# Kernel optimization log

Hardware: AMD Instinct MI355X
Metric: run time of the kernel (lower is better)

## Reference

```python
import jax, jax.numpy as jnp
import numpy as np

RNN_SIZE = 256
FC_DIM = 64
IMG_DIM = 3200
EMB_DIM = 300


def setup_inputs() -> dict:
    key = jax.random.key(0)
    ks = jax.random.split(key, 16)
    n, L = 64, 512
    s = 0.02
    return {
        "img_feats": jax.random.normal(ks[0], (n, L, IMG_DIM), jnp.float32),
        "phrase_emb": jax.random.normal(ks[1], (n, EMB_DIM), jnp.float32),
        "masks": jnp.ones((n, L), jnp.float32),
        "select_ixs": jax.random.randint(ks[2], (n,), 0, L),
        # cnn_fc_layer: Linear(3200 -> 64)
        "W_cnn": jax.random.normal(ks[3], (IMG_DIM, FC_DIM), jnp.float32) * s,
        "b_cnn": jnp.zeros((FC_DIM,), jnp.float32),
        # phrase_embed: Linear(300 -> 64)
        "W_phr": jax.random.normal(ks[4], (EMB_DIM, FC_DIM), jnp.float32) * s,
        "b_phr": jnp.zeros((FC_DIM,), jnp.float32),
        # LSTMCell(64 -> 256), gate order i,f,g,o as in torch
        "W_ih": jax.random.normal(ks[5], (FC_DIM, 4 * RNN_SIZE), jnp.float32) * s,
        "b_ih": jnp.zeros((4 * RNN_SIZE,), jnp.float32),
        "W_hh": jax.random.normal(ks[6], (RNN_SIZE, 4 * RNN_SIZE), jnp.float32) * s,
        "b_hh": jnp.zeros((4 * RNN_SIZE,), jnp.float32),
        # classifier: Linear(256 -> 64) -> ReLU -> Linear(64 -> 2) -> LogSoftmax
        "W_c1": jax.random.normal(ks[7], (RNN_SIZE, FC_DIM), jnp.float32) * s,
        "b_c1": jnp.zeros((FC_DIM,), jnp.float32),
        "W_c2": jax.random.normal(ks[8], (FC_DIM, 2), jnp.float32) * s,
        "b_c2": jnp.zeros((2,), jnp.float32),
    }


def _forward(img_feats, phrase_emb, select_ixs,
             W_cnn, b_cnn, W_phr, b_phr,
             W_ih, b_ih, W_hh, b_hh,
             W_c1, b_c1, W_c2, b_c2):
    n, L, _ = img_feats.shape
    # per-step small FCs, vectorized over time (dropout is inference no-op)
    img_fc = jax.nn.relu(jnp.einsum('nld,df->nlf', img_feats, W_cnn) + b_cnn)  # (n,L,64)
    emb = jax.nn.relu(phrase_emb @ W_phr + b_phr)                               # (n,64)
    fuse = img_fc * emb[:, None, :]                                             # (n,L,64)

    def cell(carry, x_t):
        h, c = carry
        gates = x_t @ W_ih + b_ih + h @ W_hh + b_hh        # (n, 4*H)
        i, f, g, o = jnp.split(gates, 4, axis=-1)
        i, f, o = jax.nn.sigmoid(i), jax.nn.sigmoid(f), jax.nn.sigmoid(o)
        g = jnp.tanh(g)
        c = f * c + i * g
        h = o * jnp.tanh(c)
        return (h, c), h

    h0 = jnp.zeros((n, RNN_SIZE), fuse.dtype)
    c0 = jnp.zeros((n, RNN_SIZE), fuse.dtype)
    _, hs = jax.lax.scan(cell, (h0, c0), jnp.swapaxes(fuse, 0, 1))  # (L,n,H)
    output_feats = jnp.swapaxes(hs, 0, 1)                           # (n,L,H)

    hid = jax.nn.relu(jnp.einsum('nlh,hf->nlf', output_feats, W_c1) + b_c1)
    logits = jnp.einsum('nlf,fk->nlk', hid, W_c2) + b_c2
    logprobs = jax.nn.log_softmax(logits, axis=-1)                  # (n,L,2)

    selected = jnp.take_along_axis(output_feats, select_ixs[:, None, None], axis=1)[:, 0, :]
    return logprobs, output_feats, selected


def reference(img_feats, phrase_emb, masks, select_ixs,
              W_cnn, b_cnn, W_phr, b_phr,
              W_ih, b_ih, W_hh, b_hh,
              W_c1, b_c1, W_c2, b_c2):
    # masks is accepted but unused, as in the original forward()
    return _forward(img_feats, phrase_emb, select_ixs,
                    W_cnn, b_cnn, W_phr, b_phr,
                    W_ih, b_ih, W_hh, b_hh,
                    W_c1, b_c1, W_c2, b_c2)
```

## Files before the change

### kernel.cpp

```cpp
#include <hip/hip_runtime.h>
#include <hip/hip_bf16.h>
#include <stdint.h>

#define LSEQ 512
#define NB   64
#define IMGD 3200
#define EMBD 300
#define HD   256

typedef __bf16 bf16x8 __attribute__((ext_vector_type(8)));
typedef float  f32x4  __attribute__((ext_vector_type(4)));

__device__ __forceinline__ unsigned short f2bf(float x) {
  unsigned u = __builtin_bit_cast(unsigned, x);
  u = (u + 0x7FFFu + ((u >> 16) & 1u)) >> 16;
  return (unsigned short)u;
}

__global__ __launch_bounds__(256) void k1_init_emb(
    const float* __restrict__ phr, const float* __restrict__ Wp,
    const float* __restrict__ bp, float* __restrict__ emb,
    unsigned* __restrict__ hbuf) {
  int tid = threadIdx.x, blk = blockIdx.x;
  int gid = blk * 256 + tid;
  if (gid < 16384)
    hbuf[gid] = 0u;
  if (blk < 16) {
    int b = gid >> 6, f = gid & 63;
    float acc = bp[f];
    for (int k = 0; k < EMBD; ++k) acc += phr[b * EMBD + k] * Wp[k * 64 + f];
    emb[gid] = fmaxf(acc, 0.f);
  }
}

__global__ __launch_bounds__(256) void k2_imgfuse(
    const float* __restrict__ img, const float* __restrict__ Wc,
    const float* __restrict__ bc, const float* __restrict__ emb,
    unsigned short* __restrict__ fuse) {
  __shared__ float sX[32 * 65];
  __shared__ float sW[64 * 64];
  int tid = threadIdx.x, blk = blockIdx.x;
  int r = tid & 31, g = tid >> 5;
  int rs = tid >> 3, cs = (tid & 7) * 8;
  float acc[8];
#pragma unroll
  for (int j = 0; j < 8; ++j) acc[j] = 0.f;

  for (int k0 = 0; k0 < IMGD; k0 += 64) {
    const float* xsrc = img + (size_t)(blk * 32 + rs) * IMGD + k0 + cs;
    float4 v0 = *(const float4*)xsrc;
    float4 v1 = *(const float4*)(xsrc + 4);
    float* xd = sX + rs * 65 + cs;
    xd[0]=v0.x; xd[1]=v0.y; xd[2]=v0.z; xd[3]=v0.w;
    xd[4]=v1.x; xd[5]=v1.y; xd[6]=v1.z; xd[7]=v1.w;
    const float4* wsrc = (const float4*)(Wc + k0 * 64);
#pragma unroll
    for (int i = 0; i < 4; ++i) ((float4*)sW)[i * 256 + tid] = wsrc[i * 256 + tid];
    __syncthreads();
#pragma unroll 8
    for (int k = 0; k < 64; ++k) {
      float xv = sX[r * 65 + k];
      const float* wr = sW + k * 64 + g * 8;
      float4 wa = *(const float4*)wr;
      float4 wb = *(const float4*)(wr + 4);
      acc[0] += xv * wa.x; acc[1] += xv * wa.y; acc[2] += xv * wa.z; acc[3] += xv * wa.w;
      acc[4] += xv * wb.x; acc[5] += xv * wb.y; acc[6] += xv * wb.z; acc[7] += xv * wb.w;
    }
    __syncthreads();
  }
  int rowg = blk * 32 + r;
  int b = rowg >> 9;
  unsigned pk[4];
#pragma unroll
  for (int j2 = 0; j2 < 4; ++j2) {
    int c = g * 8 + j2 * 2;
    float v0 = fmaxf(acc[j2 * 2] + bc[c], 0.f) * emb[b * 64 + c];
    float v1 = fmaxf(acc[j2 * 2 + 1] + bc[c + 1], 0.f) * emb[b * 64 + c + 1];
    pk[j2] = (unsigned)f2bf(v0) | ((unsigned)f2bf(v1) << 16);
  }
  *(uint4*)(fuse + (size_t)rowg * 64 + g * 8) = make_uint4(pk[0], pk[1], pk[2], pk[3]);
}

__global__ __launch_bounds__(256) void k3_lstm(
    const float* __restrict__ Wih, const float* __restrict__ bih,
    const float* __restrict__ Whh, const float* __restrict__ bhh,
    const unsigned short* __restrict__ fuse,
    unsigned* __restrict__ hbuf, float* __restrict__ outfeats) {
  __shared__ __align__(16) unsigned short sZ[16 * 328];
  int tid = threadIdx.x;
  int wg  = blockIdx.x;
  int grp = wg >> 4;
  int j16 = wg & 15;
  int b0  = grp * 16;
  int h0  = j16 * 16;
  int w = tid >> 6, l = tid & 63;
  int q = l >> 4, c = l & 15;

  int gcol = (c >> 2) * 256 + h0 + w * 4 + (c & 3);
  bf16x8 Bf[10];
#pragma unroll
  for (int kk = 0; kk < 10; ++kk) {
#pragma unroll
    for (int j = 0; j < 8; ++j) {
      int k = kk * 32 + q * 8 + j;
      float v = (k < 256) ? Whh[k * 1024 + gcol] : Wih[(k - 256) * 1024 + gcol];
      Bf[kk][j] = __builtin_bit_cast(__bf16, f2bf(v));
    }
  }
  float bv = bih[gcol] + bhh[gcol];

  int row = tid >> 4, u16i = tid & 15;
  const unsigned short* fbase = fuse + ((size_t)(b0 + row) * 512) * 64 + u16i * 4;
  unsigned short* zh = sZ + row * 328 + u16i * 16;
  unsigned short* zx = sZ + row * 328 + 256 + u16i * 4;
  const unsigned short* za = sZ + c * 328 + q * 8;

  int batch = (q << 2) + ((l >> 2) & 3);
  int ug = h0 + ((w << 2) | (l & 3));
  float* obase = outfeats + ((size_t)(b0 + batch) * 512) * 256 + ug;
  unsigned* mbase = hbuf + (size_t)(b0 + batch) * 256 + ug;
  float cst = 0.f;

  for (int step = 0; step < LSEQ; ++step) {
    uint2 fv = *(const uint2*)(fbase + (size_t)step * 64);
    __syncthreads();
    const unsigned long long* pb =
        (const unsigned long long*)(hbuf + (step & 1) * 16384 +
                                    (b0 + row) * 256 + u16i * 16);
    unsigned long long want = (unsigned long long)(step & 0xFFFF);
    unsigned long long m[8];
    for (;;) {
      bool ok = true;
#pragma unroll
      for (int i = 0; i < 8; ++i)
        m[i] = __hip_atomic_load(pb + i, __ATOMIC_RELAXED, __HIP_MEMORY_SCOPE_AGENT);
#pragma unroll
      for (int i = 0; i < 8; ++i)
        ok = ok && (((m[i] >> 16) & 0xFFFFull) == want) && ((m[i] >> 48) == want);
      if (ok) break;
      __builtin_amdgcn_s_sleep(1);
    }
    unsigned o0 = (unsigned)((m[0] & 0xFFFFull) | ((m[0] >> 16) & 0xFFFF0000ull));
    unsigned o1 = (unsigned)((m[1] & 0xFFFFull) | ((m[1] >> 16) & 0xFFFF0000ull));
    unsigned o2 = (unsigned)((m[2] & 0xFFFFull) | ((m[2] >> 16) & 0xFFFF0000ull));
    unsigned o3 = (unsigned)((m[3] & 0xFFFFull) | ((m[3] >> 16) & 0xFFFF0000ull));
    unsigned o4 = (unsigned)((m[4] & 0xFFFFull) | ((m[4] >> 16) & 0xFFFF0000ull));
    unsigned o5 = (unsigned)((m[5] & 0xFFFFull) | ((m[5] >> 16) & 0xFFFF0000ull));
    unsigned o6 = (unsigned)((m[6] & 0xFFFFull) | ((m[6] >> 16) & 0xFFFF0000ull));
    unsigned o7 = (unsigned)((m[7] & 0xFFFFull) | ((m[7] >> 16) & 0xFFFF0000ull));
    ((uint4*)zh)[0] = make_uint4(o0, o1, o2, o3);
    ((uint4*)zh)[1] = make_uint4(o4, o5, o6, o7);
    *(uint2*)zx = fv;
    __syncthreads();
    f32x4 acc = {bv, bv, bv, bv};
#pragma unroll
    for (int kk = 0; kk < 10; ++kk) {
      bf16x8 a = *(const bf16x8*)(za + kk * 32);
      acc = __builtin_amdgcn_mfma_f32_16x16x32_bf16(a, Bf[kk], acc, 0, 0, 0);
    }
    int g0 = (l >> 2) & 1, g1 = (l >> 3) & 1;
    float v0 = acc[0], v1 = acc[1], v2 = acc[2], v3 = acc[3];
    float s0 = __shfl_xor(v1, 4), s1 = __shfl_xor(v0, 4);
    float s2 = __shfl_xor(v3, 4), s3 = __shfl_xor(v2, 4);
    float y0 = (g0 == 0) ? v0 : s0;
    float y1 = (g0 == 1) ? v1 : s1;
    float y2 = (g0 == 0) ? v2 : s2;
    float y3 = (g0 == 1) ? v3 : s3;
    float t0 = __shfl_xor(y2, 8), t1 = __shfl_xor(y3, 8);
    float t2 = __shfl_xor(y0, 8), t3 = __shfl_xor(y1, 8);
    float zi = (g1 == 0) ? y0 : t0;
    float zf = (g1 == 0) ? y1 : t1;
    float zg = (g1 == 1) ? y2 : t2;
    float zo = (g1 == 1) ? y3 : t3;
    float si = 1.f / (1.f + __expf(-zi));
    float sf = 1.f / (1.f + __expf(-zf));
    float so = 1.f / (1.f + __expf(-zo));
    float e2g = __expf(2.f * zg);
    float tg = (e2g - 1.f) / (e2g + 1.f);
    cst = sf * cst + si * tg;
    float e2c = __expf(2.f * cst);
    float hn = so * (e2c - 1.f) / (e2c + 1.f);
    obase[(size_t)step * 256] = hn;
    unsigned pk = ((unsigned)((step + 1) & 0xFFFF) << 16) | (unsigned)f2bf(hn);
    __hip_atomic_store(mbase + (((step + 1) & 1) << 14), pk,
                       __ATOMIC_RELAXED, __HIP_MEMORY_SCOPE_AGENT);
  }
}

__global__ __launch_bounds__(256) void k4_classifier(
    const float* __restrict__ feats, const float* __restrict__ Wc1,
    const float* __restrict__ bc1, const float* __restrict__ Wc2,
    const float* __restrict__ bc2, float* __restrict__ lp) {
  __shared__ float sW[64 * 64];
  __shared__ float sX[16 * 257];
  __shared__ float sH[16 * 68];
  int tid = threadIdx.x, blk = blockIdx.x;
  {
    int rs = tid >> 4, seg = (tid & 15) * 16;
    const float4* src = (const float4*)(feats + (size_t)(blk * 16 + rs) * 256 + seg);
    float* xd = sX + rs * 257 + seg;
#pragma unroll
    for (int i = 0; i < 4; ++i) {
      float4 v = src[i];
      xd[i*4+0]=v.x; xd[i*4+1]=v.y; xd[i*4+2]=v.z; xd[i*4+3]=v.w;
    }
  }
  int r = tid & 15, g = tid >> 4;
  float acc[4] = {0.f, 0.f, 0.f, 0.f};
  for (int c4 = 0; c4 < 4; ++c4) {
    __syncthreads();
#pragma unroll
    for (int i = 0; i < 4; ++i)
      ((float4*)sW)[i * 256 + tid] = ((const float4*)(Wc1 + c4 * 4096))[i * 256 + tid];
    __syncthreads();
#pragma unroll 8
    for (int k = 0; k < 64; ++k) {
      float xv = sX[r * 257 + c4 * 64 + k];
      float4 wv = *(const float4*)(sW + k * 64 + g * 4);
      acc[0] += xv * wv.x; acc[1] += xv * wv.y; acc[2] += xv * wv.z; acc[3] += xv * wv.w;
    }
  }
#pragma unroll
  for (int j = 0; j < 4; ++j) {
    int c = g * 4 + j;
    sH[r * 68 + c] = fmaxf(acc[j] + bc1[c], 0.f);
  }
  __syncthreads();
  if (tid < 16) {
    float l0 = bc2[0], l1 = bc2[1];
    for (int c = 0; c < 64; ++c) {
      float h = sH[tid * 68 + c];
      l0 += h * Wc2[c * 2]; l1 += h * Wc2[c * 2 + 1];
    }
    float mx = fmaxf(l0, l1);
    float lse = mx + logf(__expf(l0 - mx) + __expf(l1 - mx));
    int rowg = blk * 16 + tid;
    lp[rowg * 2]     = l0 - lse;
    lp[rowg * 2 + 1] = l1 - lse;
  }
}

__global__ __launch_bounds__(256) void k5_select(
    const float* __restrict__ feats, const int* __restrict__ six,
    float* __restrict__ sel) {
  int b = blockIdx.x, tid = threadIdx.x;
  int ix = six[b];
  sel[b * 256 + tid] = feats[((size_t)b * 512 + ix) * 256 + tid];
}

extern "C" void kernel_launch(void* const* d_in, const int* in_sizes, int n_in,
                              void* d_out, int out_size, void* d_ws, size_t ws_size,
                              hipStream_t stream) {
  const float* img = (const float*)d_in[0];
  const float* phr = (const float*)d_in[1];
  const int*   six = (const int*)d_in[3];
  const float* Wc  = (const float*)d_in[4];
  const float* bc  = (const float*)d_in[5];
  const float* Wp  = (const float*)d_in[6];
  const float* bp  = (const float*)d_in[7];
  const float* Wih = (const float*)d_in[8];
  const float* bih = (const float*)d_in[9];
  const float* Whh = (const float*)d_in[10];
  const float* bhh = (const float*)d_in[11];
  const float* Wc1 = (const float*)d_in[12];
  const float* bc1 = (const float*)d_in[13];
  const float* Wc2 = (const float*)d_in[14];
  const float* bc2 = (const float*)d_in[15];

  float* out_lp   = (float*)d_out;
  float* out_feat = out_lp + 65536;
  float* out_sel  = out_feat + 8388608;

  char* ws = (char*)d_ws;
  float*          emb   = (float*)ws;
  unsigned short* fuse  = (unsigned short*)(ws + 16384);
  unsigned*       hbuf  = (unsigned*)(ws + 16384 + 4194304);

  hipLaunchKernelGGL(k1_init_emb, dim3(64), dim3(256), 0, stream,
                     phr, Wp, bp, emb, hbuf);
  hipLaunchKernelGGL(k2_imgfuse, dim3(1024), dim3(256), 0, stream,
                     img, Wc, bc, emb, fuse);
  hipLaunchKernelGGL(k3_lstm, dim3(64), dim3(256), 0, stream,
                     Wih, bih, Whh, bhh, fuse, hbuf, out_feat);
  hipLaunchKernelGGL(k4_classifier, dim3(2048), dim3(256), 0, stream,
                     out_feat, Wc1, bc1, Wc2, bc2, out_lp);
  hipLaunchKernelGGL(k5_select, dim3(64), dim3(256), 0, stream,
                     out_feat, six, out_sel);
}
```

Baseline: 2.181 ms.

## Repartition LSTM across 16 workgroups with per-gate MFMA tiles and double-buffered LDS

The LSTM recurrence now runs on 16 workgroups instead of 64. Each wave computes all four gates for 16 hidden units over 4 MFMA accumulators, which removes the cross-lane shuffles used to regroup gates. The fused Whh/Wih weights are pre-packed to bf16 in the MFMA fragment layout by the init kernel, so each workgroup loads them with vector reads. LDS is double-buffered so one barrier per step can be dropped, and the sleep in the spin-wait is removed. This reduces inter-workgroup synchronization fan-in but puts 4x more MFMA work per step on each wave and uses more registers for the weights.

```diff
diff --git a/kernel.cpp b/kernel.cpp
--- a/kernel.cpp
+++ b/kernel.cpp
@@ -7,6 +7,7 @@
 #define IMGD 3200
 #define EMBD 300
 #define HD   256
+#define KCH  10
 
 typedef __bf16 bf16x8 __attribute__((ext_vector_type(8)));
 typedef float  f32x4  __attribute__((ext_vector_type(4)));
@@ -19,12 +20,26 @@
 
 __global__ __launch_bounds__(256) void k1_init_emb(
     const float* __restrict__ phr, const float* __restrict__ Wp,
-    const float* __restrict__ bp, float* __restrict__ emb,
-    unsigned* __restrict__ hbuf) {
+    const float* __restrict__ bp, const float* __restrict__ Wih,
+    const float* __restrict__ Whh, float* __restrict__ emb,
+    unsigned* __restrict__ hbuf, unsigned short* __restrict__ Wpk) {
   int tid = threadIdx.x, blk = blockIdx.x;
   int gid = blk * 256 + tid;
   if (gid < 16384)
     hbuf[gid] = 0u;
+  for (int e = gid; e < 327680; e += 16384) {
+    int j = e & 7;
+    int t1 = e >> 3;
+    int l = t1 & 63;
+    int t2 = t1 >> 6;
+    int kk = t2 % 10;
+    int t3 = t2 / 10;
+    int g = t3 & 3, w = (t3 >> 2) & 3, j4 = t3 >> 4;
+    int k = kk * 32 + ((l >> 4) << 3) + j;
+    int col = g * 256 + j4 * 64 + w * 16 + (l & 15);
+    float v = (k < 256) ? Whh[k * 1024 + col] : Wih[(k - 256) * 1024 + col];
+    Wpk[e] = f2bf(v);
+  }
   if (blk < 16) {
     int b = gid >> 6, f = gid & 63;
     float acc = bp[f];
@@ -82,51 +97,49 @@
 }
 
 __global__ __launch_bounds__(256) void k3_lstm(
-    const float* __restrict__ Wih, const float* __restrict__ bih,
-    const float* __restrict__ Whh, const float* __restrict__ bhh,
+    const unsigned short* __restrict__ Wpk,
+    const float* __restrict__ bih, const float* __restrict__ bhh,
     const unsigned short* __restrict__ fuse,
     unsigned* __restrict__ hbuf, float* __restrict__ outfeats) {
-  __shared__ __align__(16) unsigned short sZ[16 * 328];
+  __shared__ __align__(16) unsigned short sZ[2][16 * 328];
   int tid = threadIdx.x;
   int wg  = blockIdx.x;
-  int grp = wg >> 4;
-  int j16 = wg & 15;
+  int grp = wg & 3;
+  int j4  = wg >> 2;
   int b0  = grp * 16;
-  int h0  = j16 * 16;
   int w = tid >> 6, l = tid & 63;
   int q = l >> 4, c = l & 15;
 
-  int gcol = (c >> 2) * 256 + h0 + w * 4 + (c & 3);
-  bf16x8 Bf[10];
-#pragma unroll
-  for (int kk = 0; kk < 10; ++kk) {
-#pragma unroll
-    for (int j = 0; j < 8; ++j) {
-      int k = kk * 32 + q * 8 + j;
-      float v = (k < 256) ? Whh[k * 1024 + gcol] : Wih[(k - 256) * 1024 + gcol];
-      Bf[kk][j] = __builtin_bit_cast(__bf16, f2bf(v));
-    }
-  }
-  float bv = bih[gcol] + bhh[gcol];
+  bf16x8 Bf[4][KCH];
+  const bf16x8* wp = (const bf16x8*)Wpk + (size_t)((j4 * 4 + w) * 4) * KCH * 64 + l;
+#pragma unroll
+  for (int g = 0; g < 4; ++g)
+#pragma unroll
+    for (int kk = 0; kk < KCH; ++kk)
+      Bf[g][kk] = wp[(g * KCH + kk) * 64];
+  float bv[4];
+#pragma unroll
+  for (int g = 0; g < 4; ++g) {
+    int colg = g * 256 + j4 * 64 + w * 16 + c;
+    bv[g] = bih[colg] + bhh[colg];
+  }
 
   int row = tid >> 4, u16i = tid & 15;
   const unsigned short* fbase = fuse + ((size_t)(b0 + row) * 512) * 64 + u16i * 4;
-  unsigned short* zh = sZ + row * 328 + u16i * 16;
-  unsigned short* zx = sZ + row * 328 + 256 + u16i * 4;
-  const unsigned short* za = sZ + c * 328 + q * 8;
-
-  int batch = (q << 2) + ((l >> 2) & 3);
-  int ug = h0 + ((w << 2) | (l & 3));
-  float* obase = outfeats + ((size_t)(b0 + batch) * 512) * 256 + ug;
-  unsigned* mbase = hbuf + (size_t)(b0 + batch) * 256 + ug;
-  float cst = 0.f;
+  unsigned short* zh[2] = {&sZ[0][row * 328 + u16i * 16], &sZ[1][row * 328 + u16i * 16]};
+  unsigned short* zx[2] = {&sZ[0][row * 328 + 256 + u16i * 4], &sZ[1][row * 328 + 256 + u16i * 4]};
+  const unsigned short* za[2] = {&sZ[0][c * 328 + q * 8], &sZ[1][c * 328 + q * 8]};
+
+  int u = j4 * 64 + w * 16 + c;
+  float cst[4] = {0.f, 0.f, 0.f, 0.f};
+  float* ob = outfeats + ((size_t)(b0 + q * 4) * 512) * 256 + u;
+  unsigned* mb = hbuf + (size_t)(b0 + q * 4) * 256 + u;
 
   for (int step = 0; step < LSEQ; ++step) {
+    int p = step & 1;
     uint2 fv = *(const uint2*)(fbase + (size_t)step * 64);
-    __syncthreads();
     const unsigned long long* pb =
-        (const unsigned long long*)(hbuf + (step & 1) * 16384 +
-                                    (b0 + row) * 256 + u16i * 16);
+        (const unsigned long long*)(hbuf + p * 16384 + (b0 + row) * 256 + u16i * 16);
     unsigned long long want = (unsigned long long)(step & 0xFFFF);
     unsigned long long m[8];
     for (;;) {
@@ -138,7 +151,6 @@
       for (int i = 0; i < 8; ++i)
         ok = ok && (((m[i] >> 16) & 0xFFFFull) == want) && ((m[i] >> 48) == want);
       if (ok) break;
-      __builtin_amdgcn_s_sleep(1);
     }
     unsigned o0 = (unsigned)((m[0] & 0xFFFFull) | ((m[0] >> 16) & 0xFFFF0000ull));
     unsigned o1 = (unsigned)((m[1] & 0xFFFFull) | ((m[1] >> 16) & 0xFFFF0000ull));
@@ -148,42 +160,41 @@
     unsigned o5 = (unsigned)((m[5] & 0xFFFFull) | ((m[5] >> 16) & 0xFFFF0000ull));
     unsigned o6 = (unsigned)((m[6] & 0xFFFFull) | ((m[6] >> 16) & 0xFFFF0000ull));
     unsigned o7 = (unsigned)((m[7] & 0xFFFFull) | ((m[7] >> 16) & 0xFFFF0000ull));
-    ((uint4*)zh)[0] = make_uint4(o0, o1, o2, o3);
-    ((uint4*)zh)[1] = make_uint4(o4, o5, o6, o7);
-    *(uint2*)zx = fv;
-    __syncthreads();
-    f32x4 acc = {bv, bv, bv, bv};
-#pragma unroll
-    for (int kk = 0; kk < 10; ++kk) {
-      bf16x8 a = *(const bf16x8*)(za + kk * 32);
-      acc = __builtin_amdgcn_mfma_f32_16x16x32_bf16(a, Bf[kk], acc, 0, 0, 0);
-    }
-    int g0 = (l >> 2) & 1, g1 = (l >> 3) & 1;
-    float v0 = acc[0], v1 = acc[1], v2 = acc[2], v3 = acc[3];
-    float s0 = __shfl_xor(v1, 4), s1 = __shfl_xor(v0, 4);
-    float s2 = __shfl_xor(v3, 4), s3 = __shfl_xor(v2, 4);
-    float y0 = (g0 == 0) ? v0 : s0;
-    float y1 = (g0 == 1) ? v1 : s1;
-    float y2 = (g0 == 0) ? v2 : s2;
-    float y3 = (g0 == 1) ? v3 : s3;
-    float t0 = __shfl_xor(y2, 8), t1 = __shfl_xor(y3, 8);
-    float t2 = __shfl_xor(y0, 8), t3 = __shfl_xor(y1, 8);
-    float zi = (g1 == 0) ? y0 : t0;
-    float zf = (g1 == 0) ? y1 : t1;
-    float zg = (g1 == 1) ? y2 : t2;
-    float zo = (g1 == 1) ? y3 : t3;
-    float si = 1.f / (1.f + __expf(-zi));
-    float sf = 1.f / (1.f + __expf(-zf));
-    float so = 1.f / (1.f + __expf(-zo));
-    float e2g = __expf(2.f * zg);
-    float tg = (e2g - 1.f) / (e2g + 1.f);
-    cst = sf * cst + si * tg;
-    float e2c = __expf(2.f * cst);
-    float hn = so * (e2c - 1.f) / (e2c + 1.f);
-    obase[(size_t)step * 256] = hn;
-    unsigned pk = ((unsigned)((step + 1) & 0xFFFF) << 16) | (unsigned)f2bf(hn);
-    __hip_atomic_store(mbase + (((step + 1) & 1) << 14), pk,
-                       __ATOMIC_RELAXED, __HIP_MEMORY_SCOPE_AGENT);
+    unsigned short* zhp = p ? zh[1] : zh[0];
+    ((uint4*)zhp)[0] = make_uint4(o0, o1, o2, o3);
+    ((uint4*)zhp)[1] = make_uint4(o4, o5, o6, o7);
+    *(uint2*)(p ? zx[1] : zx[0]) = fv;
+    __syncthreads();
+    const unsigned short* zap = p ? za[1] : za[0];
+    f32x4 a0 = {bv[0], bv[0], bv[0], bv[0]};
+    f32x4 a1 = {bv[1], bv[1], bv[1], bv[1]};
+    f32x4 a2 = {bv[2], bv[2], bv[2], bv[2]};
+    f32x4 a3 = {bv[3], bv[3], bv[3], bv[3]};
+#pragma unroll
+    for (int kk = 0; kk < KCH; ++kk) {
+      bf16x8 A = *(const bf16x8*)(zap + kk * 32);
+      a0 = __builtin_amdgcn_mfma_f32_16x16x32_bf16(A, Bf[0][kk], a0, 0, 0, 0);
+      a1 = __builtin_amdgcn_mfma_f32_16x16x32_bf16(A, Bf[1][kk], a1, 0, 0, 0);
+      a2 = __builtin_amdgcn_mfma_f32_16x16x32_bf16(A, Bf[2][kk], a2, 0, 0, 0);
+      a3 = __builtin_amdgcn_mfma_f32_16x16x32_bf16(A, Bf[3][kk], a3, 0, 0, 0);
+    }
+    unsigned tag = (unsigned)((step + 1) & 0xFFFF) << 16;
+    unsigned* mbp = mb + ((~step & 1) << 14);
+#pragma unroll
+    for (int r = 0; r < 4; ++r) {
+      float zi = a0[r], zf = a1[r], zg = a2[r], zo = a3[r];
+      float si = 1.f / (1.f + __expf(-zi));
+      float sf = 1.f / (1.f + __expf(-zf));
+      float so = 1.f / (1.f + __expf(-zo));
+      float e2g = __expf(2.f * zg);
+      float tg = (e2g - 1.f) / (e2g + 1.f);
+      cst[r] = sf * cst[r] + si * tg;
+      float e2c = __expf(2.f * cst[r]);
+      float hn = so * (e2c - 1.f) / (e2c + 1.f);
+      ob[((size_t)r * 512 + step) * 256] = hn;
+      __hip_atomic_store(mbp + r * 256, tag | (unsigned)f2bf(hn),
+                         __ATOMIC_RELAXED, __HIP_MEMORY_SCOPE_AGENT);
+    }
   }
 }
 
@@ -274,14 +285,15 @@
   char* ws = (char*)d_ws;
   float*          emb   = (float*)ws;
   unsigned short* fuse  = (unsigned short*)(ws + 16384);
-  unsigned*       hbuf  = (unsigned*)(ws + 16384 + 4194304);
+  unsigned*       hbuf  = (unsigned*)(ws + 4210688);
+  unsigned short* Wpk   = (unsigned short*)(ws + 4341760);
 
   hipLaunchKernelGGL(k1_init_emb, dim3(64), dim3(256), 0, stream,
-                     phr, Wp, bp, emb, hbuf);
+                     phr, Wp, bp, Wih, Whh, emb, hbuf, Wpk);
   hipLaunchKernelGGL(k2_imgfuse, dim3(1024), dim3(256), 0, stream,
                      img, Wc, bc, emb, fuse);
-  hipLaunchKernelGGL(k3_lstm, dim3(64), dim3(256), 0, stream,
-                     Wih, bih, Whh, bhh, fuse, hbuf, out_feat);
+  hipLaunchKernelGGL(k3_lstm, dim3(16), dim3(256), 0, stream,
+                     Wpk, bih, bhh, fuse, hbuf, out_feat);
   hipLaunchKernelGGL(k4_classifier, dim3(2048), dim3(256), 0, stream,
                      out_feat, Wc1, bc1, Wc2, bc2, out_lp);
   hipLaunchKernelGGL(k5_select, dim3(64), dim3(256), 0, stream,
```

Result: faster. 2.124 ms (-2.6%).
